# Optimization experiments

Measured on AMD Instinct MI355X. Metric: run time of the kernel, lower is better.

The kernel has to match this reference:

```python
import jax, jax.numpy as jnp
import numpy as np
import math

NB_STEPS = 50          # quadrature sub-intervals -> 51 Clenshaw-Curtis points
NUM_RNN_STEPS = 2


def _cc_weights(nb_steps):
    # Faithful port of UMNN's compute_cc_weights (Clenshaw-Curtis quadrature).
    lam = np.arange(0, nb_steps + 1).reshape(-1, 1).astype(np.float64)
    lam = np.cos((lam @ lam.T) * math.pi / nb_steps)
    lam[:, 0] = 0.5
    lam[:, -1] = 0.5 * lam[:, -1]
    lam = lam * 2.0 / nb_steps
    W = np.arange(0, nb_steps + 1).reshape(-1, 1).astype(np.float64)
    W[np.arange(1, nb_steps + 1, 2)] = 0
    W = 2.0 / (1.0 - W ** 2)
    W[0] = 1.0
    W[np.arange(1, nb_steps + 1, 2)] = 0
    cc = (lam.T @ W).astype(np.float32).reshape(-1)                      # [S]
    steps = np.cos(np.arange(0, nb_steps + 1) * math.pi / nb_steps).astype(np.float32)  # [S]
    return jnp.asarray(cc), jnp.asarray(steps)

CC_W, CC_STEPS = _cc_weights(NB_STEPS)  # S = NB_STEPS + 1 = 51


def _integrand(t, h, W1, b1, W2, b2, W3, b3, final_w):
    # IntegrandNN: MLP(cat(t,h)) -> ELU + 1 (>=0) -> fused power features -> ReLU(Linear)
    z = jnp.concatenate([t, h], axis=1)          # [N, in_d]
    z = jax.nn.relu(z @ W1.T + b1)               # [N, 128]
    z = jax.nn.relu(z @ W2.T + b2)               # [N, 128]
    z = jax.nn.elu(z @ W3.T + b3) + 1.0          # [N, 1], >= 0
    p = jnp.concatenate([z ** 1.5, z ** 2, z ** 2.5, z ** 3, z ** 3.5], axis=1)  # [N, 5]
    return jax.nn.relu((1.0 / (p + 1.0)) @ final_w.T)  # [N, 1]


def _inner_integral(x, h, params):
    # InnerUMNN: integral of IntegrandNN from x to xmax, xmax = max(x) + 10 (global scalar)
    N = x.shape[0]
    S = NB_STEPS + 1
    xmax = jnp.max(x) + 10.0
    T = x + (xmax - x) * (CC_STEPS[None, :] + 1.0) * 0.5   # [N, S]
    Tf = T.reshape(N * S, 1)
    hf = jnp.broadcast_to(h[:, None, :], (N, S, h.shape[1])).reshape(N * S, -1)
    g = _integrand(Tf, hf, *params).reshape(N, S)
    z = jnp.sum(g * CC_W[None, :], axis=1, keepdims=True)  # [N, 1]
    return z * (xmax - x) * 0.5


def _outer_integral(xT, h, params):
    # ParallelNeuralIntegral of InnerUMNN from x0 = 0 to xT; xT: [B, 1]
    B = xT.shape[0]
    S = NB_STEPS + 1
    X = xT * (CC_STEPS[None, :] + 1.0) * 0.5               # [B, S] (x0 = 0)
    Xf = X.reshape(B * S, 1)
    hf = jnp.broadcast_to(h[:, None, :], (B, S, h.shape[1])).reshape(B * S, -1)
    f = _inner_integral(Xf, hf, params).reshape(B, S)      # nested quadrature
    z = jnp.sum(f * CC_W[None, :], axis=1, keepdims=True)  # [B, 1]
    return z * xT * 0.5


def setup_inputs() -> dict:
    key = jax.random.key(0)
    ks = jax.random.split(key, 8)
    B, NF, IN_D, H = 256, 512, 64, 128
    x_ = jax.random.normal(ks[0], (B, NF), jnp.float32)
    h_ = jax.random.normal(ks[1], (B, IN_D - 1), jnp.float32)

    def lin(k, o, i):
        lim = 1.0 / np.sqrt(i)
        kw, kb = jax.random.split(k)
        return (jax.random.uniform(kw, (o, i), jnp.float32, -lim, lim),
                jax.random.uniform(kb, (o,), jnp.float32, -lim, lim))

    W1, b1 = lin(ks[2], H, IN_D)
    W2, b2 = lin(ks[3], H, H)
    W3, b3 = lin(ks[4], 1, H)
    lim5 = 1.0 / np.sqrt(5.0)
    final_w = jnp.abs(jax.random.uniform(ks[5], (1, 5), jnp.float32, -lim5, lim5))  # reset_params: abs
    log_weight = jnp.ones((1, NF), jnp.float32)            # reset_parameters: all ones
    sigmoid_param = jax.random.normal(ks[6], (1,), jnp.float32)
    return dict(x_=x_, h_=h_, W1=W1, b1=b1, W2=W2, b2=b2, W3=W3, b3=b3,
                final_w=final_w, log_weight=log_weight, sigmoid_param=sigmoid_param)


def reference(x_, h_, W1, b1, W2, b2, W3, b3, final_w, log_weight, sigmoid_param):
    params = (W1, b1, W2, b2, W3, b3, final_w)
    # compute_modular_function: F.linear then sum over dim 1 -> [B, 1]
    xm = jnp.sum(x_ @ log_weight.T, axis=1, keepdims=True)
    lam = jax.nn.sigmoid(sigmoid_param)                    # [1]
    out = jnp.zeros_like(xm)
    for _ in range(NUM_RNN_STEPS):
        xT = (1.0 - lam) * xm + lam * out
        out = _outer_integral(xT, h_, params)
    return out
```

## Files before the change

kernel.cpp:

```cpp
#include <hip/hip_runtime.h>
#include <math.h>

#define BB 256
#define NF 512
#define IND 64
#define HD 128
#define SS 51
#define NHM1 63

#define WS_LAM  0
#define WS_CCW  16
#define WS_U    80
#define WS_XM   144
#define WS_OUT1 656
#define WSH_C1  2048
#define WSH_W1  34816
#define WSH_W2F 40960
#define WS_W2F_F4 5120

typedef _Float16 f16x2 __attribute__((ext_vector_type(2)));
typedef __fp16   fp16x2 __attribute__((ext_vector_type(2)));
typedef _Float16 f16x8 __attribute__((ext_vector_type(8)));
typedef float    f32x16 __attribute__((ext_vector_type(16)));

union f16x8_split { f16x8 v8; f16x2 v2[4]; };
union pk_cast { fp16x2 p; f16x2 f; };

static __device__ inline f16x2 cvt_pk(float a, float b) {
    pk_cast u; u.p = __builtin_amdgcn_cvt_pkrtz(a, b);
    return u.f;
}

static __device__ inline float dot2f(f16x2 a, f16x2 b, float c) {
#if __has_builtin(__builtin_amdgcn_fdot2)
    return __builtin_amdgcn_fdot2(a, b, c, false);
#else
    return c + (float)a[0] * (float)b[0] + (float)a[1] * (float)b[1];
#endif
}

__global__ void k_setup(const float* __restrict__ x_, const float* __restrict__ h_,
                        const float* __restrict__ W1, const float* __restrict__ b1,
                        const float* __restrict__ W2, const float* __restrict__ lw,
                        const float* __restrict__ sp, float* __restrict__ ws) {
    int b = blockIdx.x;
    int j = threadIdx.x;
    short* wsh = (short*)ws;

    float acc = b1[j];
    const float* w1row = W1 + j * IND;
    const float* hrow  = h_ + b * NHM1;
    #pragma unroll 7
    for (int k = 0; k < NHM1; ++k) acc = fmaf(w1row[1 + k], hrow[k], acc);
    {
        _Float16 hv = (_Float16)acc;
        short sv; __builtin_memcpy(&sv, &hv, 2);
        wsh[WSH_C1 + b * HD + j] = sv;
    }

    float s = 0.f;
    for (int k = j; k < NF; k += HD) s = fmaf(x_[b * NF + k], lw[k], s);
    __shared__ float red[HD];
    red[j] = s;
    __syncthreads();
    for (int off = 64; off > 0; off >>= 1) {
        if (j < off) red[j] += red[j + off];
        __syncthreads();
    }
    if (j == 0) ws[WS_XM + b] = red[0];

    if (b < 128) {
        int d = b * 128 + j;
        int i = d & 7, lane = (d >> 3) & 63, kn = d >> 9;
        int kk = kn >> 2, nt = kn & 3;
        int row = nt * 32 + (lane & 31);
        int k = kk * 16 + (lane >> 5) * 8 + i;
        _Float16 hv = (_Float16)W2[row * HD + k];
        short sv; __builtin_memcpy(&sv, &hv, 2);
        wsh[WSH_W2F + d] = sv;
    }

    if (b == 0) {
        if (j < SS) {
            float acc2 = 0.f;
            for (int jj = 0; jj <= 50; jj += 2) {
                float wj = (jj == 0) ? 1.f : 2.f / (1.f - (float)(jj * jj));
                float lamv;
                if (j == 0 || j == 50) {
                    lamv = 0.02f;
                } else {
                    int m = (jj * j) % 100;
                    lamv = cosf((float)m * (float)M_PI / 50.f) * 0.04f;
                }
                acc2 = fmaf(lamv, wj, acc2);
            }
            ws[WS_CCW + j] = acc2;
            float st = cosf((float)j * (float)M_PI / 50.f);
            ws[WS_U + j] = (st + 1.f) * 0.5f;
        }
        if (j == 127) ws[WS_LAM] = 1.f / (1.f + expf(-sp[0]));
    }
    if (b == 2) {
        _Float16 hv = (_Float16)W1[j * IND];
        short sv; __builtin_memcpy(&sv, &hv, 2);
        wsh[WSH_W1 + j] = sv;
    }
    if (b == 4) ws[WS_OUT1 + j] = 0.f;
    if (b == 5) ws[WS_OUT1 + 128 + j] = 0.f;
}

__launch_bounds__(256, 2)
__global__ void k_int(const float* __restrict__ b2, const float* __restrict__ W3,
                      const float* __restrict__ b3, const float* __restrict__ fw,
                      const float* __restrict__ ws, const float* __restrict__ outprev,
                      float* __restrict__ tgt, float* __restrict__ ztgt) {
    int b = blockIdx.x >> 1, hf = blockIdx.x & 1;
    int tid = threadIdx.x;
    int wv = tid >> 6, l = tid & 63;
    int e32 = l & 31, h2 = l >> 5;

    __shared__ __align__(16) short w2s[16384];
    __shared__ __align__(16) short c1h[HD], w1h[HD];
    __shared__ float us[SS], ccs[SS], xw[4];

    if (ztgt && hf == 0 && tid == 0) ztgt[b] = 0.f;

    {
        const float4* src = reinterpret_cast<const float4*>(ws) + WS_W2F_F4;
        float4* dst = reinterpret_cast<float4*>(w2s);
        #pragma unroll
        for (int k = 0; k < 8; ++k) dst[tid + k * 256] = src[tid + k * 256];
    }
    {
        const short* wsh0 = (const short*)ws;
        if (tid < HD) { c1h[tid] = wsh0[WSH_C1 + b * HD + tid]; w1h[tid] = wsh0[WSH_W1 + tid]; }
    }
    if (tid < SS) { us[tid] = ws[WS_U + tid]; ccs[tid] = ws[WS_CCW + tid]; }

    float lam = ws[WS_LAM];
    float xmv = ws[WS_XM + tid];
    float opv = outprev ? outprev[tid] : 0.f;
    float xtv = (1.f - lam) * xmv + lam * opv;
    float mx = fmaxf(xtv, 0.f);
    #pragma unroll
    for (int off = 32; off >= 1; off >>= 1) mx = fmaxf(mx, __shfl_xor(mx, off, 64));
    if (l == 0) xw[wv] = mx;
    __syncthreads();
    float xmax = fmaxf(fmaxf(xw[0], xw[1]), fmaxf(xw[2], xw[3])) + 10.f;
    float xT = (1.f - lam) * ws[WS_XM + b] + lam * (outprev ? outprev[b] : 0.f);

    f16x2 b2pk[4][8], w3pk[4][8];
    #pragma unroll
    for (int nt = 0; nt < 4; ++nt) {
        int jb = nt * 32;
        #pragma unroll
        for (int q = 0; q < 8; ++q) {
            int r0 = ((2 * q) & 3) + 8 * ((2 * q) >> 2) + 4 * h2;
            b2pk[nt][q] = cvt_pk(b2[jb + r0], b2[jb + r0 + 1]);
            w3pk[nt][q] = cvt_pk(W3[jb + r0], W3[jb + r0 + 1]);
        }
    }
    float b3v = b3[0];
    float fw0 = fw[0], fw1 = fw[1], fw2 = fw[2], fw3 = fw[3], fw4 = fw[4];

    float accO = 0.f;
    float zs_prev = 0.f, w_prev = 0.f;
    const f16x2 z2 = {(_Float16)0.f, (_Float16)0.f};

    #pragma unroll 1
    for (int it = 0; it < 11; ++it) {
        int tl = hf * 4 + wv + it * 8;
        int m = tl * 32 + e32;
        int valid = (m <= 2600);
        int mm = valid ? m : 2600;
        int s  = (mm * 41121) >> 21;
        int si = mm - s * 51;
        float x = xT * us[s];
        float range = xmax - x;
        float t = fmaf(range, us[si], x);
        float wgt = valid ? (ccs[si] * ccs[s] * range * xT * 0.25f) : 0.f;
        float wsel = h2 ? 0.f : wgt;
        _Float16 th = (_Float16)t;
        f16x2 tv = {th, th};

        f32x16 C0, C1, C2, C3;
        #pragma unroll
        for (int e = 0; e < 16; ++e) { C0[e] = 0.f; C1[e] = 0.f; C2[e] = 0.f; C3[e] = 0.f; }

        {
            float z = zs_prev > 0.f ? zs_prev + 1.f : __expf(zs_prev);
            float sq = sqrtf(z);
            float p15 = z * sq, p2 = z * z, p25 = p2 * sq, p3 = p2 * z, p35 = p3 * sq;
            float g = fw0 * __builtin_amdgcn_rcpf(p15 + 1.f)
                    + fw1 * __builtin_amdgcn_rcpf(p2  + 1.f)
                    + fw2 * __builtin_amdgcn_rcpf(p25 + 1.f)
                    + fw3 * __builtin_amdgcn_rcpf(p3  + 1.f)
                    + fw4 * __builtin_amdgcn_rcpf(p35 + 1.f);
            g = fmaxf(g, 0.f);
            accO = fmaf(g, w_prev, accO);
        }

        #pragma unroll
        for (int kp = 0; kp < 4; ++kp) {
            __builtin_amdgcn_sched_barrier(0);
            #pragma unroll
            for (int kd = 0; kd < 2; ++kd) {
                int kk = kp * 2 + kd;
                f16x8_split c8, w8, Bu;
                c8.v8 = *reinterpret_cast<const f16x8*>(&c1h[kk * 16 + h2 * 8]);
                w8.v8 = *reinterpret_cast<const f16x8*>(&w1h[kk * 16 + h2 * 8]);
                #pragma unroll
                for (int p = 0; p < 4; ++p)
                    Bu.v2[p] = __builtin_elementwise_max(
                        __builtin_elementwise_fma(w8.v2[p], tv, c8.v2[p]), z2);
                const f16x8* Afp = reinterpret_cast<const f16x8*>(
                    &w2s[(kk * 4 * 64 + l) * 8]);
                C0 = __builtin_amdgcn_mfma_f32_32x32x16_f16(Afp[ 0], Bu.v8, C0, 0, 0, 0);
                C1 = __builtin_amdgcn_mfma_f32_32x32x16_f16(Afp[ 64], Bu.v8, C1, 0, 0, 0);
                C2 = __builtin_amdgcn_mfma_f32_32x32x16_f16(Afp[128], Bu.v8, C2, 0, 0, 0);
                C3 = __builtin_amdgcn_mfma_f32_32x32x16_f16(Afp[192], Bu.v8, C3, 0, 0, 0);
            }
        }
        __builtin_amdgcn_sched_barrier(0);

        float za = 0.f, zb = 0.f, zc = 0.f, zd = 0.f;
        #pragma unroll
        for (int q = 0; q < 8; ++q) {
            f16x2 a0 = cvt_pk(C0[2 * q], C0[2 * q + 1]);
            a0 = __builtin_elementwise_max(a0 + b2pk[0][q], z2);
            za = dot2f(a0, w3pk[0][q], za);
            f16x2 a1 = cvt_pk(C1[2 * q], C1[2 * q + 1]);
            a1 = __builtin_elementwise_max(a1 + b2pk[1][q], z2);
            zb = dot2f(a1, w3pk[1][q], zb);
            f16x2 a2 = cvt_pk(C2[2 * q], C2[2 * q + 1]);
            a2 = __builtin_elementwise_max(a2 + b2pk[2][q], z2);
            zc = dot2f(a2, w3pk[2][q], zc);
            f16x2 a3 = cvt_pk(C3[2 * q], C3[2 * q + 1]);
            a3 = __builtin_elementwise_max(a3 + b2pk[3][q], z2);
            zd = dot2f(a3, w3pk[3][q], zd);
        }
        float z1 = (za + zb) + (zc + zd);
        z1 += __shfl_xor(z1, 32, 64);
        zs_prev = z1 + b3v;
        w_prev = wsel;
    }

    {
        float z = zs_prev > 0.f ? zs_prev + 1.f : __expf(zs_prev);
        float sq = sqrtf(z);
        float p15 = z * sq, p2 = z * z, p25 = p2 * sq, p3 = p2 * z, p35 = p3 * sq;
        float g = fw0 * __builtin_amdgcn_rcpf(p15 + 1.f)
                + fw1 * __builtin_amdgcn_rcpf(p2  + 1.f)
                + fw2 * __builtin_amdgcn_rcpf(p25 + 1.f)
                + fw3 * __builtin_amdgcn_rcpf(p3  + 1.f)
                + fw4 * __builtin_amdgcn_rcpf(p35 + 1.f);
        g = fmaxf(g, 0.f);
        accO = fmaf(g, w_prev, accO);
    }

    #pragma unroll
    for (int off = 32; off >= 1; off >>= 1) accO += __shfl_xor(accO, off, 64);
    if (l == 0) atomicAdd(&tgt[b], accO);
}

extern "C" void kernel_launch(void* const* d_in, const int* in_sizes, int n_in,
                              void* d_out, int out_size, void* d_ws, size_t ws_size,
                              hipStream_t stream) {
    (void)in_sizes; (void)n_in; (void)out_size; (void)ws_size;
    const float* x_ = (const float*)d_in[0];
    const float* h_ = (const float*)d_in[1];
    const float* W1 = (const float*)d_in[2];
    const float* b1 = (const float*)d_in[3];
    const float* W2 = (const float*)d_in[4];
    const float* b2 = (const float*)d_in[5];
    const float* W3 = (const float*)d_in[6];
    const float* b3 = (const float*)d_in[7];
    const float* fw = (const float*)d_in[8];
    const float* lw = (const float*)d_in[9];
    const float* sp = (const float*)d_in[10];
    float* wsf  = (float*)d_ws;
    float* out1 = wsf + WS_OUT1;
    float* out  = (float*)d_out;

    k_setup<<<BB, HD, 0, stream>>>(x_, h_, W1, b1, W2, lw, sp, wsf);
    k_int<<<BB * 2, 256, 0, stream>>>(b2, W3, b3, fw, wsf, nullptr, out1, out);
    k_int<<<BB * 2, 256, 0, stream>>>(b2, W3, b3, fw, wsf, out1, out, nullptr);
}
```

Baseline: 75.66 us.

## Process two quadrature tiles per loop iteration to reuse W2 fragments

Unrolls the main quadrature loop by two, computing two tiles of sample points per iteration with eight accumulator sets that share the loaded W2 A-fragments. This is meant to cut LDS fragment reads per MFMA and expose more independent MFMA chains to hide latency. It adds one padded, zero-weighted extra tile (12 vs 11) and doubles accumulator register use, which may reduce occupancy.

```diff
diff --git a/kernel.cpp b/kernel.cpp
--- a/kernel.cpp
+++ b/kernel.cpp
@@ -164,31 +164,39 @@
     float fw0 = fw[0], fw1 = fw[1], fw2 = fw[2], fw3 = fw[3], fw4 = fw[4];
 
     float accO = 0.f;
-    float zs_prev = 0.f, w_prev = 0.f;
+    float zsA = 0.f, wA = 0.f, zsB = 0.f, wB = 0.f;
     const f16x2 z2 = {(_Float16)0.f, (_Float16)0.f};
 
     #pragma unroll 1
-    for (int it = 0; it < 11; ++it) {
-        int tl = hf * 4 + wv + it * 8;
-        int m = tl * 32 + e32;
-        int valid = (m <= 2600);
-        int mm = valid ? m : 2600;
-        int s  = (mm * 41121) >> 21;
-        int si = mm - s * 51;
-        float x = xT * us[s];
-        float range = xmax - x;
-        float t = fmaf(range, us[si], x);
-        float wgt = valid ? (ccs[si] * ccs[s] * range * xT * 0.25f) : 0.f;
-        float wsel = h2 ? 0.f : wgt;
-        _Float16 th = (_Float16)t;
-        f16x2 tv = {th, th};
-
-        f32x16 C0, C1, C2, C3;
-        #pragma unroll
-        for (int e = 0; e < 16; ++e) { C0[e] = 0.f; C1[e] = 0.f; C2[e] = 0.f; C3[e] = 0.f; }
+    for (int d = 0; d < 6; ++d) {
+        float t0, t1, ws0, ws1;
+        #pragma unroll
+        for (int p = 0; p < 2; ++p) {
+            int tl = hf * 4 + wv + (2 * d + p) * 8;
+            int m = tl * 32 + e32;
+            int valid = (m <= 2600);
+            int mm = valid ? m : 2600;
+            int s  = (mm * 41121) >> 21;
+            int si = mm - s * 51;
+            float x = xT * us[s];
+            float range = xmax - x;
+            float t = fmaf(range, us[si], x);
+            float wgt = valid ? (ccs[si] * ccs[s] * range * xT * 0.25f) : 0.f;
+            float wsel = h2 ? 0.f : wgt;
+            if (p == 0) { t0 = t; ws0 = wsel; } else { t1 = t; ws1 = wsel; }
+        }
+        _Float16 th0 = (_Float16)t0, th1 = (_Float16)t1;
+        f16x2 tv0 = {th0, th0}, tv1 = {th1, th1};
+
+        f32x16 C0, C1, C2, C3, C4, C5, C6, C7;
+        #pragma unroll
+        for (int e = 0; e < 16; ++e) {
+            C0[e] = 0.f; C1[e] = 0.f; C2[e] = 0.f; C3[e] = 0.f;
+            C4[e] = 0.f; C5[e] = 0.f; C6[e] = 0.f; C7[e] = 0.f;
+        }
 
         {
-            float z = zs_prev > 0.f ? zs_prev + 1.f : __expf(zs_prev);
+            float z = zsA > 0.f ? zsA + 1.f : __expf(zsA);
             float sq = sqrtf(z);
             float p15 = z * sq, p2 = z * z, p25 = p2 * sq, p3 = p2 * z, p35 = p3 * sq;
             float g = fw0 * __builtin_amdgcn_rcpf(p15 + 1.f)
@@ -196,8 +204,16 @@
                     + fw2 * __builtin_amdgcn_rcpf(p25 + 1.f)
                     + fw3 * __builtin_amdgcn_rcpf(p3  + 1.f)
                     + fw4 * __builtin_amdgcn_rcpf(p35 + 1.f);
-            g = fmaxf(g, 0.f);
-            accO = fmaf(g, w_prev, accO);
+            accO = fmaf(fmaxf(g, 0.f), wA, accO);
+            z = zsB > 0.f ? zsB + 1.f : __expf(zsB);
+            sq = sqrtf(z);
+            p15 = z * sq; p2 = z * z; p25 = p2 * sq; p3 = p2 * z; p35 = p3 * sq;
+            g = fw0 * __builtin_amdgcn_rcpf(p15 + 1.f)
+              + fw1 * __builtin_amdgcn_rcpf(p2  + 1.f)
+              + fw2 * __builtin_amdgcn_rcpf(p25 + 1.f)
+              + fw3 * __builtin_amdgcn_rcpf(p3  + 1.f)
+              + fw4 * __builtin_amdgcn_rcpf(p35 + 1.f);
+            accO = fmaf(fmaxf(g, 0.f), wB, accO);
         }
 
         #pragma unroll
@@ -206,47 +222,79 @@
             #pragma unroll
             for (int kd = 0; kd < 2; ++kd) {
                 int kk = kp * 2 + kd;
-                f16x8_split c8, w8, Bu;
+                f16x8_split c8, w8, Bu0, Bu1;
                 c8.v8 = *reinterpret_cast<const f16x8*>(&c1h[kk * 16 + h2 * 8]);
                 w8.v8 = *reinterpret_cast<const f16x8*>(&w1h[kk * 16 + h2 * 8]);
                 #pragma unroll
-                for (int p = 0; p < 4; ++p)
-                    Bu.v2[p] = __builtin_elementwise_max(
-                        __builtin_elementwise_fma(w8.v2[p], tv, c8.v2[p]), z2);
+                for (int p = 0; p < 4; ++p) {
+                    Bu0.v2[p] = __builtin_elementwise_max(
+                        __builtin_elementwise_fma(w8.v2[p], tv0, c8.v2[p]), z2);
+                    Bu1.v2[p] = __builtin_elementwise_max(
+                        __builtin_elementwise_fma(w8.v2[p], tv1, c8.v2[p]), z2);
+                }
                 const f16x8* Afp = reinterpret_cast<const f16x8*>(
                     &w2s[(kk * 4 * 64 + l) * 8]);
-                C0 = __builtin_amdgcn_mfma_f32_32x32x16_f16(Afp[ 0], Bu.v8, C0, 0, 0, 0);
-                C1 = __builtin_amdgcn_mfma_f32_32x32x16_f16(Afp[ 64], Bu.v8, C1, 0, 0, 0);
-                C2 = __builtin_amdgcn_mfma_f32_32x32x16_f16(Afp[128], Bu.v8, C2, 0, 0, 0);
-                C3 = __builtin_amdgcn_mfma_f32_32x32x16_f16(Afp[192], Bu.v8, C3, 0, 0, 0);
+                f16x8 A0 = Afp[0], A1 = Afp[64], A2 = Afp[128], A3 = Afp[192];
+                C0 = __builtin_amdgcn_mfma_f32_32x32x16_f16(A0, Bu0.v8, C0, 0, 0, 0);
+                C4 = __builtin_amdgcn_mfma_f32_32x32x16_f16(A0, Bu1.v8, C4, 0, 0, 0);
+                C1 = __builtin_amdgcn_mfma_f32_32x32x16_f16(A1, Bu0.v8, C1, 0, 0, 0);
+                C5 = __builtin_amdgcn_mfma_f32_32x32x16_f16(A1, Bu1.v8, C5, 0, 0, 0);
+                C2 = __builtin_amdgcn_mfma_f32_32x32x16_f16(A2, Bu0.v8, C2, 0, 0, 0);
+                C6 = __builtin_amdgcn_mfma_f32_32x32x16_f16(A2, Bu1.v8, C6, 0, 0, 0);
+                C3 = __builtin_amdgcn_mfma_f32_32x32x16_f16(A3, Bu0.v8, C3, 0, 0, 0);
+                C7 = __builtin_amdgcn_mfma_f32_32x32x16_f16(A3, Bu1.v8, C7, 0, 0, 0);
             }
         }
         __builtin_amdgcn_sched_barrier(0);
 
-        float za = 0.f, zb = 0.f, zc = 0.f, zd = 0.f;
-        #pragma unroll
-        for (int q = 0; q < 8; ++q) {
-            f16x2 a0 = cvt_pk(C0[2 * q], C0[2 * q + 1]);
-            a0 = __builtin_elementwise_max(a0 + b2pk[0][q], z2);
-            za = dot2f(a0, w3pk[0][q], za);
-            f16x2 a1 = cvt_pk(C1[2 * q], C1[2 * q + 1]);
-            a1 = __builtin_elementwise_max(a1 + b2pk[1][q], z2);
-            zb = dot2f(a1, w3pk[1][q], zb);
-            f16x2 a2 = cvt_pk(C2[2 * q], C2[2 * q + 1]);
-            a2 = __builtin_elementwise_max(a2 + b2pk[2][q], z2);
-            zc = dot2f(a2, w3pk[2][q], zc);
-            f16x2 a3 = cvt_pk(C3[2 * q], C3[2 * q + 1]);
-            a3 = __builtin_elementwise_max(a3 + b2pk[3][q], z2);
-            zd = dot2f(a3, w3pk[3][q], zd);
-        }
-        float z1 = (za + zb) + (zc + zd);
-        z1 += __shfl_xor(z1, 32, 64);
-        zs_prev = z1 + b3v;
-        w_prev = wsel;
+        {
+            float za = 0.f, zb = 0.f, zc = 0.f, zd = 0.f;
+            #pragma unroll
+            for (int q = 0; q < 8; ++q) {
+                f16x2 a0 = cvt_pk(C0[2 * q], C0[2 * q + 1]);
+                a0 = __builtin_elementwise_max(a0 + b2pk[0][q], z2);
+                za = dot2f(a0, w3pk[0][q], za);
+                f16x2 a1 = cvt_pk(C1[2 * q], C1[2 * q + 1]);
+                a1 = __builtin_elementwise_max(a1 + b2pk[1][q], z2);
+                zb = dot2f(a1, w3pk[1][q], zb);
+                f16x2 a2 = cvt_pk(C2[2 * q], C2[2 * q + 1]);
+                a2 = __builtin_elementwise_max(a2 + b2pk[2][q], z2);
+                zc = dot2f(a2, w3pk[2][q], zc);
+                f16x2 a3 = cvt_pk(C3[2 * q], C3[2 * q + 1]);
+                a3 = __builtin_elementwise_max(a3 + b2pk[3][q], z2);
+                zd = dot2f(a3, w3pk[3][q], zd);
+            }
+            float z1 = (za + zb) + (zc + zd);
+            z1 += __shfl_xor(z1, 32, 64);
+            zsA = z1 + b3v;
+            wA = ws0;
+        }
+        {
+            float za = 0.f, zb = 0.f, zc = 0.f, zd = 0.f;
+            #pragma unroll
+            for (int q = 0; q < 8; ++q) {
+                f16x2 a0 = cvt_pk(C4[2 * q], C4[2 * q + 1]);
+                a0 = __builtin_elementwise_max(a0 + b2pk[0][q], z2);
+                za = dot2f(a0, w3pk[0][q], za);
+                f16x2 a1 = cvt_pk(C5[2 * q], C5[2 * q + 1]);
+                a1 = __builtin_elementwise_max(a1 + b2pk[1][q], z2);
+                zb = dot2f(a1, w3pk[1][q], zb);
+                f16x2 a2 = cvt_pk(C6[2 * q], C6[2 * q + 1]);
+                a2 = __builtin_elementwise_max(a2 + b2pk[2][q], z2);
+                zc = dot2f(a2, w3pk[2][q], zc);
+                f16x2 a3 = cvt_pk(C7[2 * q], C7[2 * q + 1]);
+                a3 = __builtin_elementwise_max(a3 + b2pk[3][q], z2);
+                zd = dot2f(a3, w3pk[3][q], zd);
+            }
+            float z1 = (za + zb) + (zc + zd);
+            z1 += __shfl_xor(z1, 32, 64);
+            zsB = z1 + b3v;
+            wB = ws1;
+        }
     }
 
     {
-        float z = zs_prev > 0.f ? zs_prev + 1.f : __expf(zs_prev);
+        float z = zsA > 0.f ? zsA + 1.f : __expf(zsA);
         float sq = sqrtf(z);
         float p15 = z * sq, p2 = z * z, p25 = p2 * sq, p3 = p2 * z, p35 = p3 * sq;
         float g = fw0 * __builtin_amdgcn_rcpf(p15 + 1.f)
@@ -254,8 +302,16 @@
                 + fw2 * __builtin_amdgcn_rcpf(p25 + 1.f)
                 + fw3 * __builtin_amdgcn_rcpf(p3  + 1.f)
                 + fw4 * __builtin_amdgcn_rcpf(p35 + 1.f);
-        g = fmaxf(g, 0.f);
-        accO = fmaf(g, w_prev, accO);
+        accO = fmaf(fmaxf(g, 0.f), wA, accO);
+        z = zsB > 0.f ? zsB + 1.f : __expf(zsB);
+        sq = sqrtf(z);
+        p15 = z * sq; p2 = z * z; p25 = p2 * sq; p3 = p2 * z; p35 = p3 * sq;
+        g = fw0 * __builtin_amdgcn_rcpf(p15 + 1.f)
+          + fw1 * __builtin_amdgcn_rcpf(p2  + 1.f)
+          + fw2 * __builtin_amdgcn_rcpf(p25 + 1.f)
+          + fw3 * __builtin_amdgcn_rcpf(p3  + 1.f)
+          + fw4 * __builtin_amdgcn_rcpf(p35 + 1.f);
+        accO = fmaf(fmaxf(g, 0.f), wB, accO);
     }
 
     #pragma unroll
```

Result: no change. 74.77 us (-1.2%).
